# Performance work log

Hardware: AMD Instinct MI355X
Metric: run time of the kernel (lower is better)

Reference implementation:

```python
import jax, jax.numpy as jnp
import numpy as np
import math

D_MODEL = 1024
N_HEADS = 16
HEAD_DIM = D_MODEL // N_HEADS
THETA = 10000.0


def _rope(x, cos, sin):
    # x: [b, h, s, head_dim]; cos/sin: [s, head_dim//2]
    xe = x[..., 0::2]
    xo = x[..., 1::2]
    re = xe * cos - xo * sin
    ro = xe * sin + xo * cos
    # interleave back to even/odd layout
    return jnp.stack([re, ro], axis=-1).reshape(x.shape)


def setup_inputs() -> dict:
    key = jax.random.key(0)
    k1, k2, k3, k4, k5 = jax.random.split(key, 5)
    std = math.sqrt(2.0 / (D_MODEL + D_MODEL))
    x = jax.random.normal(k1, (2, 2048, D_MODEL), dtype=jnp.float32)
    Wq = jax.random.normal(k2, (D_MODEL, D_MODEL), dtype=jnp.float32) * std
    Wk = jax.random.normal(k3, (D_MODEL, D_MODEL), dtype=jnp.float32) * std
    Wv = jax.random.normal(k4, (D_MODEL, D_MODEL), dtype=jnp.float32) * std
    Wo = jax.random.normal(k5, (D_MODEL, D_MODEL), dtype=jnp.float32) * (std / math.sqrt(2))
    return {"x": x, "Wq": Wq, "Wk": Wk, "Wv": Wv, "Wo": Wo}


def reference(x, Wq, Wk, Wv, Wo):
    b, s, d = x.shape
    h, hd = N_HEADS, HEAD_DIM
    # projections: einsum 'batch seq d_in, d_model d_in -> batch seq d_model' == x @ W.T
    def proj(W):
        y = jnp.einsum('bsd,md->bsm', x, W)
        return y.reshape(b, s, h, hd).transpose(0, 2, 1, 3)  # [b, h, s, hd]
    Q, K, V = proj(Wq), proj(Wk), proj(Wv)
    # RoPE with default positions = arange(seq)
    freqs = 1.0 / (THETA ** (jnp.arange(0, hd, 2, dtype=jnp.float32) / hd))
    angles = jnp.arange(s, dtype=jnp.float32)[:, None] * freqs[None, :]  # [s, hd//2]
    cos, sin = jnp.cos(angles), jnp.sin(angles)
    Q = _rope(Q, cos, sin)
    K = _rope(K, cos, sin)
    # naive causal attention
    scores = jnp.einsum('bhqd,bhkd->bhqk', Q, K) / math.sqrt(hd)
    causal = jnp.tril(jnp.ones((s, s), dtype=bool))
    scores = jnp.where(causal, scores, -jnp.inf)
    attn = jax.nn.softmax(scores, axis=-1)
    out = jnp.einsum('bhqk,bhkd->bhqd', attn, V)
    out = out.transpose(0, 2, 1, 3).reshape(b, s, d)
    return jnp.einsum('bsd,md->bsm', out, Wo)
```

## Files before the change

### kernel.cpp

```cpp
#include <hip/hip_runtime.h>
#include <stdint.h>
#include <stddef.h>

typedef __bf16 bf16;
typedef __bf16 bf16x8 __attribute__((ext_vector_type(8)));
typedef __bf16 bf16x4 __attribute__((ext_vector_type(4)));
typedef short short4v __attribute__((ext_vector_type(4)));
typedef float f32x4 __attribute__((ext_vector_type(4)));

#define GAS __attribute__((address_space(1)))
#define LAS __attribute__((address_space(3)))

__device__ __forceinline__ void async_load16(const void* g, void* l) {
  __builtin_amdgcn_global_load_lds((const GAS void*)g, (LAS void*)l, 16, 0, 0);
}

__device__ __forceinline__ f32x4 mfma16(bf16x4 a, bf16x4 b, f32x4 c) {
#if defined(__HIP_DEVICE_COMPILE__)
#if __has_builtin(__builtin_amdgcn_mfma_f32_16x16x16bf16_1k)
  return __builtin_amdgcn_mfma_f32_16x16x16bf16_1k(
      __builtin_bit_cast(short4v, a), __builtin_bit_cast(short4v, b), c, 0, 0, 0);
#else
  f32x4 d;
  asm volatile("v_mfma_f32_16x16x16_bf16 %0, %1, %2, %3"
               : "=v"(d)
               : "v"(a), "v"(b), "v"(c));
  return d;
#endif
#else
  (void)a; (void)b;
  return c;
#endif
}

__global__ __launch_bounds__(256) void cast_all(
    const float* __restrict__ x, const float* __restrict__ Wq,
    const float* __restrict__ Wk, const float* __restrict__ Wv,
    const float* __restrict__ Wo, bf16* __restrict__ Xh,
    bf16* __restrict__ Wqkv, bf16* __restrict__ Woh,
    float2* __restrict__ rope) {
  if (blockIdx.x >= 8192) {
    const int e = ((blockIdx.x - 8192) * 256 + threadIdx.x) * 4;
    const int s = e >> 5, ip0 = e & 31;
#pragma unroll
    for (int r = 0; r < 4; ++r) {
      const float freq = __expf((float)(ip0 + r) * -0.2878231366242557f);
      float sn, cs;
      __sincosf((float)s * freq, &sn, &cs);
      rope[e + r] = make_float2(cs, sn);
    }
    return;
  }
  int idx = (blockIdx.x * 256 + threadIdx.x) * 4;
  const float* src;
  bf16* dst;
  float scale = 1.0f;
  if (idx < 4194304) {
    src = x + idx; dst = Xh + idx;
  } else if (idx < 7340032) {
    int j = idx - 4194304;
    if (j < 1048576) {
      src = Wq + j; scale = 0.18033688011112042f;
    } else {
      src = ((j < 2097152) ? Wk : Wv) + (j & 1048575);
    }
    dst = Wqkv + j;
  } else {
    int j = idx - 7340032;
    src = Wo + j; dst = Woh + j;
  }
  float4 v = *(const float4*)src;
  bf16x4 o;
  o[0] = (bf16)(v.x * scale); o[1] = (bf16)(v.y * scale);
  o[2] = (bf16)(v.z * scale); o[3] = (bf16)(v.w * scale);
  *(bf16x4*)dst = o;
}

__global__ __launch_bounds__(256, 3) void gemm_qkv(
    const bf16* __restrict__ A, const bf16* __restrict__ B,
    const float2* __restrict__ rope, bf16* __restrict__ Qh,
    bf16* __restrict__ Kh, bf16* __restrict__ Vt, int K) {
  __shared__ __align__(16) bf16 As[128 * 64];
  __shared__ __align__(16) bf16 Bs[128 * 64];
  const int tid = threadIdx.x;
  const int wave = tid >> 6, lane = tid & 63;
  const int bm = blockIdx.y * 128, bn = blockIdx.x * 128;
  const int wm = (wave >> 1) * 64, wn = (wave & 1) * 64;
  const int fr = lane & 15, g = lane >> 4;
  const int sw8 = (fr & 7) * 8;

  const int srow = tid >> 3;
  const int scol = 8 * ((tid & 7) ^ (srow & 7));
  const int ldst = wave * 512;

  f32x4 acc[4][4] = {};

  for (int kt = 0; kt < K; kt += 64) {
    __syncthreads();
#pragma unroll
    for (int s = 0; s < 4; ++s) {
      const int row = s * 32 + srow;
      async_load16(A + (size_t)(bm + row) * K + kt + scol,
                   (void*)(As + s * 2048 + ldst));
      async_load16(B + (size_t)(bn + row) * K + kt + scol,
                   (void*)(Bs + s * 2048 + ldst));
    }
    __syncthreads();

#pragma unroll
    for (int ks = 0; ks < 2; ++ks) {
      bf16x8 af[4], bfr[4];
      const int kq = (ks * 32 + g * 8) ^ sw8;
#pragma unroll
      for (int i = 0; i < 4; ++i)
        af[i] = *(const bf16x8*)&As[(wm + i * 16 + fr) * 64 + kq];
#pragma unroll
      for (int j = 0; j < 4; ++j)
        bfr[j] = *(const bf16x8*)&Bs[(wn + j * 16 + fr) * 64 + kq];
#pragma unroll
      for (int i = 0; i < 4; ++i)
#pragma unroll
        for (int j = 0; j < 4; ++j)
          acc[i][j] = __builtin_amdgcn_mfma_f32_16x16x32_bf16(af[i], bfr[j],
                                                              acc[i][j], 0, 0, 0);
    }
  }

  const int r0 = (lane >> 4) * 4, cc = lane & 15;
  const bool oddl = cc & 1;
#pragma unroll
  for (int i = 0; i < 4; ++i) {
    const int row0 = bm + wm + i * 16 + r0;
    const int b = row0 >> 11, s0 = row0 & 2047;
#pragma unroll
    for (int j = 0; j < 4; ++j) {
      const int col = bn + wn + j * 16 + cc;
      if (col < 2048) {
        const int hcol = col & 1023;
        const int h = hcol >> 6, d = hcol & 63;
        const int ip = d >> 1;
        const bool isK = col >= 1024;
        bf16* dst = (isK ? Kh : Qh) + ((size_t)(b * 16 + h) * 2048) * 64;
#pragma unroll
        for (int r = 0; r < 4; ++r) {
          float own = acc[i][j][r];
          float oth = __shfl_xor(own, 1, 64);
          const float2 t = rope[((s0 + r) << 5) + ip];
          float res = oddl ? (oth * t.y + own * t.x) : (own * t.x - oth * t.y);
          const int dd = isK ? (d ^ (((s0 + r) & 7) << 3)) : d;
          dst[(size_t)(s0 + r) * 64 + dd] = (bf16)res;
        }
      } else {
        const int v = col - 2048, h = v >> 6, d = v & 63;
        bf16x4 o;
#pragma unroll
        for (int r = 0; r < 4; ++r) o[r] = (bf16)acc[i][j][r];
        const int s2 = (s0 & ~63) | ((s0 ^ ((d & 7) << 3)) & 63);
        *(bf16x4*)&Vt[(((size_t)b * 16 + h) * 64 + d) * 2048 + s2] = o;
      }
    }
  }
}

template <typename OutT, int BM, int BN>
__global__ __launch_bounds__(256) void gemm_bt(
    const bf16* __restrict__ A, const bf16* __restrict__ B,
    OutT* __restrict__ C, int M, int N, int K) {
  constexpr int FM = BM / 32, FN = BN / 32;
  constexpr int SA = BM / 32, SB = BN / 32;
  __shared__ __align__(16) bf16 As[BM * 64];
  __shared__ __align__(16) bf16 Bs[BN * 64];
  const int tid = threadIdx.x;
  const int wave = tid >> 6, lane = tid & 63;
  const int bm = blockIdx.y * BM, bn = blockIdx.x * BN;
  const int wm = (wave >> 1) * (BM / 2), wn = (wave & 1) * (BN / 2);
  const int fr = lane & 15, g = lane >> 4;
  const int sw8 = (fr & 7) * 8;
  const int srow = tid >> 3;
  const int scol = 8 * ((tid & 7) ^ (srow & 7));
  const int ldst = wave * 512;

  f32x4 acc[FM][FN] = {};

  for (int kt = 0; kt < K; kt += 64) {
    __syncthreads();
#pragma unroll
    for (int s = 0; s < SA; ++s)
      async_load16(A + (size_t)(bm + s * 32 + srow) * K + kt + scol,
                   (void*)(As + s * 2048 + ldst));
#pragma unroll
    for (int s = 0; s < SB; ++s)
      async_load16(B + (size_t)(bn + s * 32 + srow) * K + kt + scol,
                   (void*)(Bs + s * 2048 + ldst));
    __syncthreads();

#pragma unroll
    for (int ks = 0; ks < 2; ++ks) {
      const int kq = (ks * 32 + g * 8) ^ sw8;
      bf16x8 af[FM], bfr[FN];
#pragma unroll
      for (int i = 0; i < FM; ++i)
        af[i] = *(const bf16x8*)&As[(wm + i * 16 + fr) * 64 + kq];
#pragma unroll
      for (int j = 0; j < FN; ++j)
        bfr[j] = *(const bf16x8*)&Bs[(wn + j * 16 + fr) * 64 + kq];
#pragma unroll
      for (int i = 0; i < FM; ++i)
#pragma unroll
        for (int j = 0; j < FN; ++j)
          acc[i][j] = __builtin_amdgcn_mfma_f32_16x16x32_bf16(af[i], bfr[j],
                                                              acc[i][j], 0, 0, 0);
    }
  }

  const int r0 = (lane >> 4) * 4, cc = lane & 15;
#pragma unroll
  for (int i = 0; i < FM; ++i)
#pragma unroll
    for (int j = 0; j < FN; ++j)
#pragma unroll
      for (int r = 0; r < 4; ++r)
        C[(size_t)(bm + wm + i * 16 + r0 + r) * N + (bn + wn + j * 16 + cc)] =
            (OutT)acc[i][j][r];
}

__global__ __launch_bounds__(256, 2) void attn(const bf16* __restrict__ Qh,
                                               const bf16* __restrict__ Kh,
                                               const bf16* __restrict__ Vt,
                                               bf16* __restrict__ Oh) {
  __shared__ __align__(16) bf16 Ks[3][64 * 64];
  __shared__ __align__(16) bf16 Vs[4][64 * 64];
  const int f = blockIdx.x;
  const int xcd = f & 7, u = (f >> 3) & 31, v = f >> 8;
  const int bh = xcd + 8 * (u & 3);
  const int j = v ? (u >> 2) : 15 - (u >> 2);
  const int tid = threadIdx.x, w = tid >> 6, lane = tid & 63;
  const int nlo = lane & 15, g = lane >> 4;
  const int q0 = j * 128, qw0 = q0 + w * 32;
  const bf16* __restrict__ Qp = Qh + (size_t)bh * 131072;
  const bf16* __restrict__ Kp = Kh + (size_t)bh * 131072;
  const bf16* __restrict__ Vp = Vt + (size_t)bh * 131072;
  const int n = 2 * (j + 1);
  const int nw = 2 * j + (w >> 1) + 1;

  bf16x8 aq[2][2];
#pragma unroll
  for (int qb = 0; qb < 2; ++qb)
#pragma unroll
    for (int ks = 0; ks < 2; ++ks)
      aq[qb][ks] =
          *(const bf16x8*)&Qp[(size_t)(qw0 + qb * 16 + nlo) * 64 + ks * 32 + g * 8];

  f32x4 oacc[2][4] = {};
  float lsum[2] = {0.f, 0.f};
  const int sw = (nlo & 7) << 3;

  const int srow = w * 16 + (lane >> 3);
  const int soff = (lane & 7) * 8;

  auto stage = [&](int i) {
    const int kbase = i * 64, sk = i % 3, sv = i & 3;
    async_load16(Kp + (size_t)(kbase + srow) * 64 + soff,
                 (void*)(Ks[sk] + w * 1024));
    async_load16(Kp + (size_t)(kbase + srow + 8) * 64 + soff,
                 (void*)(Ks[sk] + w * 1024 + 512));
    async_load16(Vp + (size_t)srow * 2048 + kbase + soff,
                 (void*)(Vs[sv] + w * 1024));
    async_load16(Vp + (size_t)(srow + 8) * 2048 + kbase + soff,
                 (void*)(Vs[sv] + w * 1024 + 512));
  };

  bf16x8 pk[4][2];
  auto rdK = [&](int slot) {
    const bf16* __restrict__ Kw = Ks[slot];
#pragma unroll
    for (int ni = 0; ni < 4; ++ni)
#pragma unroll
      for (int ks = 0; ks < 2; ++ks)
        pk[ni][ks] =
            *(const bf16x8*)&Kw[(ni * 16 + nlo) * 64 + ((ks * 32 + g * 8) ^ sw)];
  };

  bf16x4 av[4][4];
  auto rdV = [&](int slot) {
    const bf16* __restrict__ Vw = Vs[slot];
#pragma unroll
    for (int ni = 0; ni < 4; ++ni)
#pragma unroll
      for (int mi = 0; mi < 4; ++mi)
        av[ni][mi] =
            *(const bf16x4*)&Vw[(mi * 16 + nlo) * 64 + ((ni * 16 + g * 4) ^ sw)];
  };

  f32x4 st[2][4];
  auto qk = [&]() {
#pragma unroll
    for (int qb = 0; qb < 2; ++qb) {
#pragma unroll
      for (int ni = 0; ni < 4; ++ni) st[qb][ni] = f32x4{0.f, 0.f, 0.f, 0.f};
#pragma unroll
      for (int ks = 0; ks < 2; ++ks)
#pragma unroll
        for (int ni = 0; ni < 4; ++ni)
          st[qb][ni] = __builtin_amdgcn_mfma_f32_16x16x32_bf16(
              pk[ni][ks], aq[qb][ks], st[qb][ni], 0, 0, 0);
    }
  };

  bf16x4 p[2][4];
  auto expv = [&](int i) {
    const int kbase = i * 64;
    const bool dg = (i == nw - 1);
#pragma unroll
    for (int qb = 0; qb < 2; ++qb) {
      const int qg = qw0 + qb * 16 + nlo;
      if (!dg) {
#pragma unroll
        for (int ni = 0; ni < 4; ++ni)
#pragma unroll
          for (int r = 0; r < 4; ++r) {
            float e = __builtin_amdgcn_exp2f(st[qb][ni][r]);
            lsum[qb] += e;
            p[qb][ni][r] = (bf16)e;
          }
      } else {
#pragma unroll
        for (int ni = 0; ni < 4; ++ni) {
          const int kg0 = kbase + ni * 16 + g * 4;
#pragma unroll
          for (int r = 0; r < 4; ++r) {
            float e = __builtin_amdgcn_exp2f(st[qb][ni][r]);
            e = (kg0 + r <= qg) ? e : 0.0f;
            lsum[qb] += e;
            p[qb][ni][r] = (bf16)e;
          }
        }
      }
    }
  };

  auto pv = [&]() {
#pragma unroll
    for (int ni = 0; ni < 4; ++ni)
#pragma unroll
      for (int mi = 0; mi < 4; ++mi)
#pragma unroll
        for (int qb = 0; qb < 2; ++qb)
          oacc[qb][mi] = mfma16(av[ni][mi], p[qb][ni], oacc[qb][mi]);
  };

  stage(0);
  stage(1);
  asm volatile("s_waitcnt vmcnt(4)" ::: "memory");
  __builtin_amdgcn_s_barrier();

  for (int i = 0; i < n; ++i) {
    if (i + 2 < n) stage(i + 2);
    const bool doQK = (i < nw);
    const bool doPV = (i > 0);
    if (doQK) rdK(i % 3);
    if (doPV) rdV((i - 1) & 3);
    __builtin_amdgcn_s_setprio(1);
    if (doQK) qk();
    if (doPV) pv();
    __builtin_amdgcn_s_setprio(0);
    if (doQK) expv(i);
    if (i + 2 < n)
      asm volatile("s_waitcnt vmcnt(4)" ::: "memory");
    else
      asm volatile("s_waitcnt vmcnt(0)" ::: "memory");
    __builtin_amdgcn_s_barrier();
  }

  if (nw == n) {
    rdV((n - 1) & 3);
    pv();
  }

#pragma unroll
  for (int qb = 0; qb < 2; ++qb) {
    lsum[qb] += __shfl_xor(lsum[qb], 16, 64);
    lsum[qb] += __shfl_xor(lsum[qb], 32, 64);
  }

  const int bb = bh >> 4, hd = bh & 15;
#pragma unroll
  for (int qb = 0; qb < 2; ++qb) {
    const float inv = 1.0f / lsum[qb];
    const int q = qw0 + qb * 16 + nlo;
#pragma unroll
    for (int mi = 0; mi < 4; ++mi) {
      bf16x4 o;
#pragma unroll
      for (int r = 0; r < 4; ++r) o[r] = (bf16)(oacc[qb][mi][r] * inv);
      *(bf16x4*)&Oh[((size_t)bb * 2048 + q) * 1024 + hd * 64 + mi * 16 + g * 4] = o;
    }
  }
}

extern "C" void kernel_launch(void* const* d_in, const int* in_sizes, int n_in,
                              void* d_out, int out_size, void* d_ws, size_t ws_size,
                              hipStream_t stream) {
  (void)in_sizes; (void)n_in; (void)out_size; (void)ws_size;
  const float* x = (const float*)d_in[0];
  const float* Wq = (const float*)d_in[1];
  const float* Wk = (const float*)d_in[2];
  const float* Wv = (const float*)d_in[3];
  const float* Wo = (const float*)d_in[4];
  float* out = (float*)d_out;
  char* ws = (char*)d_ws;

  bf16* Xh    = (bf16*)(ws);
  bf16* Wqkv  = (bf16*)(ws + 8388608);
  bf16* Woh   = (bf16*)(ws + 14680064);
  bf16* Qh    = (bf16*)(ws + 16777216);
  bf16* Kh    = (bf16*)(ws + 25165824);
  bf16* Vt    = (bf16*)(ws + 33554432);
  bf16* Oh    = (bf16*)(ws + 41943040);
  float2* rope = (float2*)(ws + 50331648);

  cast_all<<<8256, 256, 0, stream>>>(x, Wq, Wk, Wv, Wo, Xh, Wqkv, Woh, rope);
  gemm_qkv<<<dim3(24, 32), 256, 0, stream>>>(Xh, Wqkv, rope, Qh, Kh, Vt, 1024);
  attn<<<512, 256, 0, stream>>>(Qh, Kh, Vt, Oh);
  gemm_bt<float, 128, 128><<<dim3(8, 32), 256, 0, stream>>>(Oh, Woh, out, 4096, 1024, 1024);
}
```

Measured before the change: 182.9 us.

## Replace LDS-staged attention with per-wave direct global loads and paired query tiles

```diff
diff --git a/kernel.cpp b/kernel.cpp
--- a/kernel.cpp
+++ b/kernel.cpp
@@ -147,16 +147,14 @@
           float oth = __shfl_xor(own, 1, 64);
           const float2 t = rope[((s0 + r) << 5) + ip];
           float res = oddl ? (oth * t.y + own * t.x) : (own * t.x - oth * t.y);
-          const int dd = isK ? (d ^ (((s0 + r) & 7) << 3)) : d;
-          dst[(size_t)(s0 + r) * 64 + dd] = (bf16)res;
+          dst[(size_t)(s0 + r) * 64 + d] = (bf16)res;
         }
       } else {
         const int v = col - 2048, h = v >> 6, d = v & 63;
         bf16x4 o;
 #pragma unroll
         for (int r = 0; r < 4; ++r) o[r] = (bf16)acc[i][j][r];
-        const int s2 = (s0 & ~63) | ((s0 ^ ((d & 7) << 3)) & 63);
-        *(bf16x4*)&Vt[(((size_t)b * 16 + h) * 64 + d) * 2048 + s2] = o;
+        *(bf16x4*)&Vt[(((size_t)b * 16 + h) * 64 + d) * 2048 + s0] = o;
       }
     }
   }
@@ -224,176 +222,139 @@
             (OutT)acc[i][j][r];
 }
 
-__global__ __launch_bounds__(256, 2) void attn(const bf16* __restrict__ Qh,
+__global__ __launch_bounds__(256, 1) void attn(const bf16* __restrict__ Qh,
                                                const bf16* __restrict__ Kh,
                                                const bf16* __restrict__ Vt,
                                                bf16* __restrict__ Oh) {
-  __shared__ __align__(16) bf16 Ks[3][64 * 64];
-  __shared__ __align__(16) bf16 Vs[4][64 * 64];
   const int f = blockIdx.x;
-  const int xcd = f & 7, u = (f >> 3) & 31, v = f >> 8;
-  const int bh = xcd + 8 * (u & 3);
-  const int j = v ? (u >> 2) : 15 - (u >> 2);
+  const int bh = f & 31;
   const int tid = threadIdx.x, w = tid >> 6, lane = tid & 63;
+  const int P = ((f >> 5) << 2) | w;
   const int nlo = lane & 15, g = lane >> 4;
-  const int q0 = j * 128, qw0 = q0 + w * 32;
   const bf16* __restrict__ Qp = Qh + (size_t)bh * 131072;
   const bf16* __restrict__ Kp = Kh + (size_t)bh * 131072;
   const bf16* __restrict__ Vp = Vt + (size_t)bh * 131072;
-  const int n = 2 * (j + 1);
-  const int nw = 2 * j + (w >> 1) + 1;
+  const int bb = bh >> 4, hd = bh & 15;
 
   bf16x8 aq[2][2];
-#pragma unroll
-  for (int qb = 0; qb < 2; ++qb)
-#pragma unroll
-    for (int ks = 0; ks < 2; ++ks)
-      aq[qb][ks] =
-          *(const bf16x8*)&Qp[(size_t)(qw0 + qb * 16 + nlo) * 64 + ks * 32 + g * 8];
-
-  f32x4 oacc[2][4] = {};
-  float lsum[2] = {0.f, 0.f};
-  const int sw = (nlo & 7) << 3;
-
-  const int srow = w * 16 + (lane >> 3);
-  const int soff = (lane & 7) * 8;
-
-  auto stage = [&](int i) {
-    const int kbase = i * 64, sk = i % 3, sv = i & 3;
-    async_load16(Kp + (size_t)(kbase + srow) * 64 + soff,
-                 (void*)(Ks[sk] + w * 1024));
-    async_load16(Kp + (size_t)(kbase + srow + 8) * 64 + soff,
-                 (void*)(Ks[sk] + w * 1024 + 512));
-    async_load16(Vp + (size_t)srow * 2048 + kbase + soff,
-                 (void*)(Vs[sv] + w * 1024));
-    async_load16(Vp + (size_t)(srow + 8) * 2048 + kbase + soff,
-                 (void*)(Vs[sv] + w * 1024 + 512));
+  bf16x8 pk[4][2];
+  bf16x4 avA[4][4], avB[4][4];
+
+  auto ldK = [&](int i) {
+#pragma unroll
+    for (int ni = 0; ni < 4; ++ni)
+#pragma unroll
+      for (int ks = 0; ks < 2; ++ks)
+        pk[ni][ks] = *(const bf16x8*)&Kp[(size_t)(i * 64 + ni * 16 + nlo) * 64 +
+                                         ks * 32 + g * 8];
   };
-
-  bf16x8 pk[4][2];
-  auto rdK = [&](int slot) {
-    const bf16* __restrict__ Kw = Ks[slot];
+  auto ldV = [&](bf16x4 (&dst)[4][4], int i) {
 #pragma unroll
     for (int ni = 0; ni < 4; ++ni)
 #pragma unroll
+      for (int mi = 0; mi < 4; ++mi)
+        dst[ni][mi] = *(const bf16x4*)&Vp[(size_t)(mi * 16 + nlo) * 2048 +
+                                          i * 64 + ni * 16 + g * 4];
+  };
+
+  for (int ph = 0; ph < 2; ++ph) {
+    const int qt = ph ? P : 63 - P;
+    const int n = (qt >> 1) + 1;
+    const int q0 = qt * 32;
+
+#pragma unroll
+    for (int qb = 0; qb < 2; ++qb)
+#pragma unroll
       for (int ks = 0; ks < 2; ++ks)
-        pk[ni][ks] =
-            *(const bf16x8*)&Kw[(ni * 16 + nlo) * 64 + ((ks * 32 + g * 8) ^ sw)];
-  };
-
-  bf16x4 av[4][4];
-  auto rdV = [&](int slot) {
-    const bf16* __restrict__ Vw = Vs[slot];
-#pragma unroll
-    for (int ni = 0; ni < 4; ++ni)
-#pragma unroll
-      for (int mi = 0; mi < 4; ++mi)
-        av[ni][mi] =
-            *(const bf16x4*)&Vw[(mi * 16 + nlo) * 64 + ((ni * 16 + g * 4) ^ sw)];
-  };
-
-  f32x4 st[2][4];
-  auto qk = [&]() {
-#pragma unroll
-    for (int qb = 0; qb < 2; ++qb) {
-#pragma unroll
-      for (int ni = 0; ni < 4; ++ni) st[qb][ni] = f32x4{0.f, 0.f, 0.f, 0.f};
-#pragma unroll
-      for (int ks = 0; ks < 2; ++ks)
-#pragma unroll
-        for (int ni = 0; ni < 4; ++ni)
-          st[qb][ni] = __builtin_amdgcn_mfma_f32_16x16x32_bf16(
-              pk[ni][ks], aq[qb][ks], st[qb][ni], 0, 0, 0);
-    }
-  };
-
-  bf16x4 p[2][4];
-  auto expv = [&](int i) {
-    const int kbase = i * 64;
-    const bool dg = (i == nw - 1);
-#pragma unroll
-    for (int qb = 0; qb < 2; ++qb) {
-      const int qg = qw0 + qb * 16 + nlo;
-      if (!dg) {
-#pragma unroll
-        for (int ni = 0; ni < 4; ++ni)
-#pragma unroll
-          for (int r = 0; r < 4; ++r) {
-            float e = __builtin_amdgcn_exp2f(st[qb][ni][r]);
-            lsum[qb] += e;
-            p[qb][ni][r] = (bf16)e;
-          }
-      } else {
-#pragma unroll
-        for (int ni = 0; ni < 4; ++ni) {
-          const int kg0 = kbase + ni * 16 + g * 4;
-#pragma unroll
-          for (int r = 0; r < 4; ++r) {
-            float e = __builtin_amdgcn_exp2f(st[qb][ni][r]);
-            e = (kg0 + r <= qg) ? e : 0.0f;
-            lsum[qb] += e;
-            p[qb][ni][r] = (bf16)e;
+        aq[qb][ks] =
+            *(const bf16x8*)&Qp[(size_t)(q0 + qb * 16 + nlo) * 64 + ks * 32 + g * 8];
+
+    f32x4 oacc[2][4] = {};
+    float lsum[2] = {0.f, 0.f};
+
+    ldK(0);
+    ldV(avA, 0);
+
+    auto iter = [&](int i, bf16x4 (&avCur)[4][4], bf16x4 (&avNxt)[4][4]) {
+      asm volatile("s_waitcnt vmcnt(0)" ::: "memory");
+      f32x4 st[2][4] = {};
+#pragma unroll
+      for (int qb = 0; qb < 2; ++qb)
+#pragma unroll
+        for (int ks = 0; ks < 2; ++ks)
+#pragma unroll
+          for (int ni = 0; ni < 4; ++ni)
+            st[qb][ni] = __builtin_amdgcn_mfma_f32_16x16x32_bf16(
+                pk[ni][ks], aq[qb][ks], st[qb][ni], 0, 0, 0);
+      if (i + 1 < n) {
+        ldK(i + 1);
+        ldV(avNxt, i + 1);
+      }
+      const int kbase = i * 64;
+      const bool dg = (i == n - 1);
+      bf16x4 p[2][4];
+#pragma unroll
+      for (int qb = 0; qb < 2; ++qb) {
+        const int qg = q0 + qb * 16 + nlo;
+        if (!dg) {
+#pragma unroll
+          for (int ni = 0; ni < 4; ++ni)
+#pragma unroll
+            for (int r = 0; r < 4; ++r) {
+              float e = __builtin_amdgcn_exp2f(st[qb][ni][r]);
+              lsum[qb] += e;
+              p[qb][ni][r] = (bf16)e;
+            }
+        } else {
+#pragma unroll
+          for (int ni = 0; ni < 4; ++ni) {
+            const int kg0 = kbase + ni * 16 + g * 4;
+#pragma unroll
+            for (int r = 0; r < 4; ++r) {
+              float e = __builtin_amdgcn_exp2f(st[qb][ni][r]);
+              e = (kg0 + r <= qg) ? e : 0.0f;
+              lsum[qb] += e;
+              p[qb][ni][r] = (bf16)e;
+            }
           }
         }
       }
-    }
-  };
-
-  auto pv = [&]() {
-#pragma unroll
-    for (int ni = 0; ni < 4; ++ni)
-#pragma unroll
-      for (int mi = 0; mi < 4; ++mi)
-#pragma unroll
-        for (int qb = 0; qb < 2; ++qb)
-          oacc[qb][mi] = mfma16(av[ni][mi], p[qb][ni], oacc[qb][mi]);
-  };
-
-  stage(0);
-  stage(1);
-  asm volatile("s_waitcnt vmcnt(4)" ::: "memory");
-  __builtin_amdgcn_s_barrier();
-
-  for (int i = 0; i < n; ++i) {
-    if (i + 2 < n) stage(i + 2);
-    const bool doQK = (i < nw);
-    const bool doPV = (i > 0);
-    if (doQK) rdK(i % 3);
-    if (doPV) rdV((i - 1) & 3);
-    __builtin_amdgcn_s_setprio(1);
-    if (doQK) qk();
-    if (doPV) pv();
-    __builtin_amdgcn_s_setprio(0);
-    if (doQK) expv(i);
-    if (i + 2 < n)
-      asm volatile("s_waitcnt vmcnt(4)" ::: "memory");
-    else
-      asm volatile("s_waitcnt vmcnt(0)" ::: "memory");
-    __builtin_amdgcn_s_barrier();
-  }
-
-  if (nw == n) {
-    rdV((n - 1) & 3);
-    pv();
-  }
-
-#pragma unroll
-  for (int qb = 0; qb < 2; ++qb) {
-    lsum[qb] += __shfl_xor(lsum[qb], 16, 64);
-    lsum[qb] += __shfl_xor(lsum[qb], 32, 64);
-  }
-
-  const int bb = bh >> 4, hd = bh & 15;
-#pragma unroll
-  for (int qb = 0; qb < 2; ++qb) {
-    const float inv = 1.0f / lsum[qb];
-    const int q = qw0 + qb * 16 + nlo;
-#pragma unroll
-    for (int mi = 0; mi < 4; ++mi) {
-      bf16x4 o;
-#pragma unroll
-      for (int r = 0; r < 4; ++r) o[r] = (bf16)(oacc[qb][mi][r] * inv);
-      *(bf16x4*)&Oh[((size_t)bb * 2048 + q) * 1024 + hd * 64 + mi * 16 + g * 4] = o;
+#pragma unroll
+      for (int ni = 0; ni < 4; ++ni)
+#pragma unroll
+        for (int mi = 0; mi < 4; ++mi)
+#pragma unroll
+          for (int qb = 0; qb < 2; ++qb)
+            oacc[qb][mi] = mfma16(avCur[ni][mi], p[qb][ni], oacc[qb][mi]);
+    };
+
+    int i = 0;
+    while (true) {
+      iter(i, avA, avB);
+      ++i;
+      if (i >= n) break;
+      iter(i, avB, avA);
+      ++i;
+      if (i >= n) break;
+    }
+
+#pragma unroll
+    for (int qb = 0; qb < 2; ++qb) {
+      lsum[qb] += __shfl_xor(lsum[qb], 16, 64);
+      lsum[qb] += __shfl_xor(lsum[qb], 32, 64);
+    }
+
+#pragma unroll
+    for (int qb = 0; qb < 2; ++qb) {
+      const float inv = 1.0f / lsum[qb];
+      const int q = q0 + qb * 16 + nlo;
+#pragma unroll
+      for (int mi = 0; mi < 4; ++mi) {
+        bf16x4 o;
+#pragma unroll
+        for (int r = 0; r < 4; ++r) o[r] = (bf16)(oacc[qb][mi][r] * inv);
+        *(bf16x4*)&Oh[((size_t)bb * 2048 + q) * 1024 + hd * 64 + mi * 16 + g * 4] = o;
+      }
     }
   }
 }
@@ -421,6 +382,6 @@
 
   cast_all<<<8256, 256, 0, stream>>>(x, Wq, Wk, Wv, Wo, Xh, Wqkv, Woh, rope);
   gemm_qkv<<<dim3(24, 32), 256, 0, stream>>>(Xh, Wqkv, rope, Qh, Kh, Vt, 1024);
-  attn<<<512, 256, 0, stream>>>(Qh, Kh, Vt, Oh);
+  attn<<<256, 256, 0, stream>>>(Qh, Kh, Vt, Oh);
   gemm_bt<float, 128, 128><<<dim3(8, 32), 256, 0, stream>>>(Oh, Woh, out, 4096, 1024, 1024);
 }
```

Result: slower. 228.3 us (+24.8%).
